# Kernel optimization log

Hardware: AMD Instinct MI355X
Metric: run time of the kernel (lower is better)

The kernel has to match this reference:

```python
import jax, jax.numpy as jnp
import numpy as np

N = 50000
E = 1600000
F_IN = 503
F_H = 128
NEG_SLOPE = 0.2


def setup_inputs() -> dict:
    key = jax.random.key(0)
    ks = jax.random.split(key, 24)
    s = 0.05
    inp = {
        "x": jax.random.normal(ks[0], (N, F_IN), jnp.float32),
        "edge_index": jax.random.randint(ks[1], (2, E), 0, N, jnp.int64),
        "edge_attr": jax.random.uniform(ks[2], (E, 1), jnp.float32),
        "input_mask": jax.random.uniform(ks[3], (N, 1), jnp.float32),
        # GATConv layer 1 (in=503, out=128, heads=1, edge_dim=1)
        "W1": jax.random.normal(ks[4], (F_IN, F_H), jnp.float32) * s,
        "b1": jnp.zeros((F_H,), jnp.float32),
        "as1": jax.random.normal(ks[5], (F_H,), jnp.float32) * s,
        "ad1": jax.random.normal(ks[6], (F_H,), jnp.float32) * s,
        "We1": jax.random.normal(ks[7], (1, F_H), jnp.float32) * s,
        "ae1": jax.random.normal(ks[8], (F_H,), jnp.float32) * s,
        # GATConv layer 2 (in=128, out=128)
        "W2": jax.random.normal(ks[9], (F_H, F_H), jnp.float32) * s,
        "b2": jnp.zeros((F_H,), jnp.float32),
        "as2": jax.random.normal(ks[10], (F_H,), jnp.float32) * s,
        "ad2": jax.random.normal(ks[11], (F_H,), jnp.float32) * s,
        "We2": jax.random.normal(ks[12], (1, F_H), jnp.float32) * s,
        "ae2": jax.random.normal(ks[13], (F_H,), jnp.float32) * s,
        # edge/node heads
        "Wb": jax.random.normal(ks[14], (F_H, 1), jnp.float32) * s,
        "bb": jnp.zeros((1,), jnp.float32),
        "Ww": jax.random.normal(ks[15], (F_H, 1), jnp.float32) * s,
        "bw": jnp.zeros((1,), jnp.float32),
    }
    return inp


def _gat_conv(x, src, dst, ea, W, b, a_src_vec, a_dst_vec, We, a_edge_vec):
    """PyG GATConv, heads=1, add_self_loops=True, fill_value='mean'."""
    n = x.shape[0]
    loop = jnp.arange(n)
    # self-loop edge attrs = mean of incoming edge attrs (0 if none)
    deg = jax.ops.segment_sum(jnp.ones(dst.shape, ea.dtype), dst, num_segments=n)
    ea_loop = jax.ops.segment_sum(ea, dst, num_segments=n) / jnp.maximum(deg, 1.0)[:, None]
    s = jnp.concatenate([src, loop])
    d = jnp.concatenate([dst, loop])
    ea2 = jnp.concatenate([ea, ea_loop], axis=0)  # [E+N, 1]

    h = x @ W                              # [N, F_H]
    a_s = h @ a_src_vec                    # [N]
    a_d = h @ a_dst_vec                    # [N]
    a_e = (ea2 @ We) @ a_edge_vec          # [E+N]

    alpha = jax.nn.leaky_relu(a_s[s] + a_d[d] + a_e, NEG_SLOPE)
    # scatter-softmax over destination neighborhoods (every node has a self loop)
    m = jax.lax.stop_gradient(jax.ops.segment_max(alpha, d, num_segments=n))
    ex = jnp.exp(alpha - m[d])
    den = jax.ops.segment_sum(ex, d, num_segments=n)
    coef = ex / den[d]                     # [E+N]

    out = jax.ops.segment_sum(coef[:, None] * h[s], d, num_segments=n)
    return out + b


def reference(x, edge_index, edge_attr, input_mask,
              W1, b1, as1, ad1, We1, ae1,
              W2, b2, as2, ad2, We2, ae2,
              Wb, bb, Ww, bw):
    src, dst = edge_index[0], edge_index[1]
    h = jax.nn.relu(_gat_conv(x, src, dst, edge_attr, W1, b1, as1, ad1, We1, ae1))
    h = jax.nn.relu(_gat_conv(h, src, dst, edge_attr, W2, b2, as2, ad2, We2, ae2))
    b_out = (h @ Wb + bb) * input_mask          # [N, 1]
    # directed graph: is_directed() is True, so use all edges
    w = ((h[src] + h[dst]) * 0.5) @ Ww + bw     # [E, 1]
    return (w, b_out)
```

## Files before the change

### kernel.cpp

```cpp
#include <hip/hip_runtime.h>
#include <hip/hip_fp16.h>

#define FH 128
#define NEG_SLOPE 0.2f
#define GBM 64
#define GBK 64
#define HT 1024
#define TB 8
#define NWMAX 12512
#define XLS 515


typedef _Float16 f16x8 __attribute__((ext_vector_type(8)));
typedef float f32x4 __attribute__((ext_vector_type(4)));

__global__ __launch_bounds__(HT) void hist_kernel(const int* __restrict__ ei,
                                                  unsigned short* __restrict__ hist,
                                                  int E, int N) {
  __shared__ unsigned int lh[NWMAX];
  const int b = blockIdx.x, tid = threadIdx.x;
  const int nw = (N + 3) >> 2;
  for (int j = tid; j < nw; j += HT) lh[j] = 0u;
  __syncthreads();
  const int i0 = b * (HT * TB) + tid * TB;
  if (i0 + TB <= E) {
    int4 da = *(const int4*)&ei[E + i0];
    int4 db = *(const int4*)&ei[E + i0 + 4];
    int dv[8] = {da.x, da.y, da.z, da.w, db.x, db.y, db.z, db.w};
    #pragma unroll
    for (int k = 0; k < 8; k++)
      atomicAdd(&lh[dv[k] >> 2], 1u << ((dv[k] & 3) * 8));
  } else {
    for (int i = i0; i < E; i++) {
      int d = ei[E + i];
      atomicAdd(&lh[d >> 2], 1u << ((d & 3) * 8));
    }
  }
  __syncthreads();
  unsigned short* hb = hist + (size_t)b * N;
  for (int j = tid; j < nw; j += HT) {
    unsigned v = lh[j];
    int bin = j * 4;
    if (bin + 3 < N) {
      ushort4 o;
      o.x = v & 255u; o.y = (v >> 8) & 255u; o.z = (v >> 16) & 255u; o.w = v >> 24;
      *(ushort4*)&hb[bin] = o;
    } else {
      for (int k = 0; k < 4 && bin + k < N; k++) hb[bin + k] = (v >> (k * 8)) & 255u;
    }
  }
}

__global__ void colscan_kernel(unsigned short* __restrict__ hist,
                               int* __restrict__ cnt, int N, int NBr) {
  int bin = blockIdx.x * 256 + threadIdx.x;
  if (bin >= N) return;
  int s = 0, b = 0;
  for (; b + 8 <= NBr; b += 8) {
    int t[8];
    #pragma unroll
    for (int k = 0; k < 8; k++) t[k] = hist[(size_t)(b + k) * N + bin];
    #pragma unroll
    for (int k = 0; k < 8; k++) {
      hist[(size_t)(b + k) * N + bin] = (unsigned short)s;
      s += t[k];
    }
  }
  for (; b < NBr; b++) {
    int t = hist[(size_t)b * N + bin];
    hist[(size_t)b * N + bin] = (unsigned short)s;
    s += t;
  }
  cnt[bin] = s;
}

__global__ void scan_blocksum(const int* __restrict__ deg, int* __restrict__ bsum, int n) {
  __shared__ int sm[256];
  int i = blockIdx.x * 256 + threadIdx.x;
  sm[threadIdx.x] = (i < n) ? deg[i] : 0;
  __syncthreads();
  for (int off = 128; off > 0; off >>= 1) {
    if (threadIdx.x < off) sm[threadIdx.x] += sm[threadIdx.x + off];
    __syncthreads();
  }
  if (threadIdx.x == 0) bsum[blockIdx.x] = sm[0];
}

__global__ void scan_bsum(int* __restrict__ bsum, int nb, int* __restrict__ rowptr, int N) {
  __shared__ int sm[1024];
  int t = threadIdx.x;
  int v = (t < nb) ? bsum[t] : 0;
  sm[t] = v;
  __syncthreads();
  for (int off = 1; off < 1024; off <<= 1) {
    int u = (t >= off) ? sm[t - off] : 0;
    __syncthreads();
    sm[t] += u;
    __syncthreads();
  }
  if (t < nb) bsum[t] = sm[t] - v;
  if (t == 1023) rowptr[N] = sm[1023];
}

__global__ void scan_final(const int* __restrict__ deg, const int* __restrict__ bsum,
                           int* __restrict__ rowptr, int n) {
  __shared__ int sm[256];
  int i = blockIdx.x * 256 + threadIdx.x;
  int v = (i < n) ? deg[i] : 0;
  sm[threadIdx.x] = v;
  __syncthreads();
  for (int off = 1; off < 256; off <<= 1) {
    int u = (threadIdx.x >= off) ? sm[threadIdx.x - off] : 0;
    __syncthreads();
    sm[threadIdx.x] += u;
    __syncthreads();
  }
  if (i < n) rowptr[i] = bsum[blockIdx.x] + sm[threadIdx.x] - v;
}

__global__ __launch_bounds__(HT) void place_kernel(const int* __restrict__ ei,
                                                   const float* __restrict__ ea,
                                                   const int* __restrict__ rowptr,
                                                   const unsigned short* __restrict__ off,
                                                   unsigned int* __restrict__ pack,
                                                   int E, int N) {
  __shared__ unsigned int lc[NWMAX];
  const int b = blockIdx.x, tid = threadIdx.x;
  const int nw = (N + 3) >> 2;
  for (int j = tid; j < nw; j += HT) lc[j] = 0u;
  __syncthreads();
  const unsigned short* __restrict__ ob = off + (size_t)b * N;
  const int i0 = b * (HT * TB) + tid * TB;
  if (i0 + TB <= E) {
    int4 sa = *(const int4*)&ei[i0];
    int4 sb = *(const int4*)&ei[i0 + 4];
    int4 da = *(const int4*)&ei[E + i0];
    int4 db = *(const int4*)&ei[E + i0 + 4];
    float4 aa = *(const float4*)&ea[i0];
    float4 ab = *(const float4*)&ea[i0 + 4];
    int sv[8] = {sa.x, sa.y, sa.z, sa.w, sb.x, sb.y, sb.z, sb.w};
    int dv[8] = {da.x, da.y, da.z, da.w, db.x, db.y, db.z, db.w};
    float av[8] = {aa.x, aa.y, aa.z, aa.w, ab.x, ab.y, ab.z, ab.w};
    unsigned rr[8];
    #pragma unroll
    for (int k = 0; k < 8; k++)
      rr[k] = atomicAdd(&lc[dv[k] >> 2], 1u << ((dv[k] & 3) * 8));
    int pos[8];
    #pragma unroll
    for (int k = 0; k < 8; k++)
      pos[k] = rowptr[dv[k]] + (int)ob[dv[k]] + (int)((rr[k] >> ((dv[k] & 3) * 8)) & 255u);
    #pragma unroll
    for (int k = 0; k < 8; k++)
      pack[pos[k]] = ((unsigned)sv[k] << 16) | __half_as_ushort(__float2half(av[k]));
  } else {
    for (int i = i0; i < E; i++) {
      int d = ei[E + i];
      unsigned r = atomicAdd(&lc[d >> 2], 1u << ((d & 3) * 8));
      int local = (r >> ((d & 3) * 8)) & 255;
      int pos = rowptr[d] + (int)ob[d] + local;
      pack[pos] = ((unsigned)ei[i] << 16) | __half_as_ushort(__float2half(ea[i]));
    }
  }
}

__global__ void cvec_kernel(const float* __restrict__ We1, const float* __restrict__ ae1,
                            const float* __restrict__ We2, const float* __restrict__ ae2,
                            float* __restrict__ cv) {
  int l = threadIdx.x;
  float s1 = We1[l] * ae1[l] + We1[l + 64] * ae1[l + 64];
  float s2 = We2[l] * ae2[l] + We2[l + 64] * ae2[l + 64];
  for (int off = 32; off; off >>= 1) { s1 += __shfl_down(s1, off); s2 += __shfl_down(s2, off); }
  if (l == 0) { cv[0] = s1; cv[1] = s2; }
}

__global__ void wcvt_kernel(const float* __restrict__ W, __half* __restrict__ Wt,
                            int K, int Kpad, int perm) {
  int idx = blockIdx.x * 256 + threadIdx.x;
  if (idx >= 128 * Kpad) return;
  int n = idx / Kpad, p = idx - n * Kpad;
  int k = perm ? ((p & 7) * 16 + (p >> 3)) : p;
  Wt[idx] = (k < K) ? __float2half(W[(size_t)k * 128 + n]) : __float2half(0.f);
}

__global__ __launch_bounds__(256) void xpack_kernel(const float* __restrict__ X,
                                                    __half* __restrict__ A16,
                                                    int K, int Kpad) {
  __shared__ float Ls[16 * XLS];
  const int mg = blockIdx.x, tid = threadIdx.x;
  const int nq = Kpad >> 3;
  const int total = 16 * K;
  const float* __restrict__ Xb = X + (size_t)mg * total;
  for (int i = tid; i < total; i += 256) {
    int row = i / K;
    Ls[row * XLS + (i - row * K)] = Xb[i];
  }
  {
    int npad = 16 * (Kpad - K);
    for (int i = tid; i < npad; i += 256) {
      int row = i / (Kpad - K);
      Ls[row * XLS + K + (i - row * (Kpad - K))] = 0.f;
    }
  }
  __syncthreads();
  _Float16* dst = (_Float16*)A16 + (size_t)mg * nq * 128;
  const int nfr = nq * 16;
  for (int c = tid; c < nfr; c += 256) {
    int q = c >> 4, r = c & 15;
    const float* src = &Ls[r * XLS + q * 8];
    f16x8 v;
    #pragma unroll
    for (int j = 0; j < 8; j++) v[j] = (_Float16)src[j];
    *(f16x8*)&dst[(size_t)c * 8] = v;
  }
}

__global__ __launch_bounds__(256, 4) void mfma_gemm_kernel(
    const __half* __restrict__ A16_, const __half* __restrict__ Wt_,
    const float* __restrict__ avs, const float* __restrict__ avd,
    __half* __restrict__ H16, float* __restrict__ a_s, float* __restrict__ a_d,
    int M, int Kpad) {
  __shared__ _Float16 Bl[2 * 8 * 64 * 8];
  const _Float16* __restrict__ A16 = (const _Float16*)A16_;
  const _Float16* __restrict__ Wt  = (const _Float16*)Wt_;
  const int tid  = threadIdx.x;
  const int lane = tid & 63;
  const int w    = tid >> 6;
  const int m0   = blockIdx.x * GBM;
  const int nq   = Kpad >> 3;

  f32x4 acc[8];
  #pragma unroll
  for (int i = 0; i < 8; i++) acc[i] = (f32x4){0.f, 0.f, 0.f, 0.f};

  const int mgc = min(m0 / 16 + w, M / 16 - 1);
  const _Float16* __restrict__ Abase =
      A16 + (size_t)mgc * nq * 128 + (lane >> 4) * 128 + (lane & 15) * 8;

  const int sg = tid & 7, snb = tid >> 3;

  for (int k0 = 0; k0 < Kpad; k0 += GBK) {
    #pragma unroll
    for (int i = 0; i < 4; i++) {
      int n = snb + 32 * i;
      f16x8 v = *(const f16x8*)(Wt + (size_t)n * Kpad + k0 + sg * 8);
      int kt = sg >> 2, nt = n >> 4;
      int fl = (n & 15) + (sg & 3) * 16;
      *(f16x8*)&Bl[((kt * 8 + nt) * 64 + fl) * 8] = v;
    }
    __syncthreads();
    #pragma unroll
    for (int kt = 0; kt < 2; kt++) {
      f16x8 af = *(const f16x8*)(Abase + (size_t)k0 * 16 + kt * 512);
      #pragma unroll
      for (int nt = 0; nt < 8; nt++) {
        f16x8 bf = *(const f16x8*)&Bl[((kt * 8 + nt) * 64 + lane) * 8];
        acc[nt] = __builtin_amdgcn_mfma_f32_16x16x32_f16(af, bf, acc[nt], 0, 0, 0);
      }
    }
    __syncthreads();
  }

  const int rbase = m0 + w * 16 + (lane >> 4) * 4;
  const int col   = lane & 15;
  float as_v[8], ad_v[8];
  #pragma unroll
  for (int nt = 0; nt < 8; nt++) {
    as_v[nt] = avs[nt * 16 + col];
    ad_v[nt] = avd[nt * 16 + col];
  }
  #pragma unroll
  for (int r = 0; r < 4; r++) {
    int gm = rbase + r;
    float ps = 0.f, pd = 0.f;
    #pragma unroll
    for (int nt = 0; nt < 8; nt++) {
      ps += acc[nt][r] * as_v[nt];
      pd += acc[nt][r] * ad_v[nt];
    }
    #pragma unroll
    for (int msk = 1; msk < 16; msk <<= 1) {
      ps += __shfl_xor(ps, msk);
      pd += __shfl_xor(pd, msk);
    }
    if (gm < M) {
      __half2 h0 = __floats2half2_rn(acc[0][r], acc[1][r]);
      __half2 h1 = __floats2half2_rn(acc[2][r], acc[3][r]);
      __half2 h2 = __floats2half2_rn(acc[4][r], acc[5][r]);
      __half2 h3 = __floats2half2_rn(acc[6][r], acc[7][r]);
      uint4 u;
      u.x = *(unsigned*)&h0; u.y = *(unsigned*)&h1;
      u.z = *(unsigned*)&h2; u.w = *(unsigned*)&h3;
      *(uint4*)&H16[(size_t)gm * FH + col * 8] = u;
      if (col == 0) { a_s[gm] = ps; a_d[gm] = pd; }
    }
  }
}

template<int OUTP>
__global__ __launch_bounds__(256) void agg_kernel(
    const __half* __restrict__ H16, const int* __restrict__ rowptr,
    const unsigned int* __restrict__ pack,
    const float* __restrict__ a_s, const float* __restrict__ a_d,
    const float* __restrict__ cv, int cidx,
    const float* __restrict__ bias,
    __half* __restrict__ HoutP,
    const float* __restrict__ Wb, const float* __restrict__ bb,
    const float* __restrict__ Ww, const float* __restrict__ mask,
    float* __restrict__ bout, float* __restrict__ pbuf, int N) {
  const int node = (blockIdx.x * 256 + threadIdx.x) >> 6;
  const int lane = threadIdx.x & 63;
  const int slot = lane >> 4, sl = lane & 15;
  if (node >= N) return;
  const _Float16* __restrict__ Hh = (const _Float16*)H16;
  const float c   = cv[cidx];
  const float adn = a_d[node];
  const int beg = rowptr[node], end = rowptr[node + 1];

  float acc[8] = {0.f, 0.f, 0.f, 0.f, 0.f, 0.f, 0.f, 0.f};
  float accB[8] = {0.f, 0.f, 0.f, 0.f, 0.f, 0.f, 0.f, 0.f};
  float den = 0.f, ea_tot = 0.f, denB = 0.f, eaB = 0.f;

  int p = beg + slot;
  for (; p + 4 < end; p += 8) {
    unsigned w0 = pack[p], w1 = pack[p + 4];
    int s0 = w0 >> 16, s1 = w1 >> 16;
    float e0 = __half2float(__ushort_as_half((unsigned short)(w0 & 0xffff)));
    float e1 = __half2float(__ushort_as_half((unsigned short)(w1 & 0xffff)));
    float as0 = a_s[s0], as1 = a_s[s1];
    f16x8 h0 = *(const f16x8*)(Hh + (size_t)s0 * FH + sl * 8);
    f16x8 h1 = *(const f16x8*)(Hh + (size_t)s1 * FH + sl * 8);
    float al0 = as0 + adn + c * e0;
    float al1 = as1 + adn + c * e1;
    al0 = fmaxf(al0, NEG_SLOPE * al0);
    al1 = fmaxf(al1, NEG_SLOPE * al1);
    float ex0 = __expf(al0), ex1 = __expf(al1);
    ea_tot += e0; eaB += e1;
    den += ex0; denB += ex1;
    #pragma unroll
    for (int j = 0; j < 8; j++) {
      acc[j]  += ex0 * (float)h0[j];
      accB[j] += ex1 * (float)h1[j];
    }
  }
  for (; p < end; p += 4) {
    unsigned w0 = pack[p];
    int s0 = w0 >> 16;
    float e0 = __half2float(__ushort_as_half((unsigned short)(w0 & 0xffff)));
    float al = a_s[s0] + adn + c * e0;
    al = fmaxf(al, NEG_SLOPE * al);
    float ex = __expf(al);
    f16x8 h = *(const f16x8*)(Hh + (size_t)s0 * FH + sl * 8);
    ea_tot += e0;
    den += ex;
    #pragma unroll
    for (int j = 0; j < 8; j++) acc[j] += ex * (float)h[j];
  }
  den += denB; ea_tot += eaB;
  #pragma unroll
  for (int j = 0; j < 8; j++) acc[j] += accB[j];
  ea_tot += __shfl_xor(ea_tot, 16); ea_tot += __shfl_xor(ea_tot, 32);
  den    += __shfl_xor(den,    16); den    += __shfl_xor(den,    32);
  #pragma unroll
  for (int j = 0; j < 8; j++) {
    acc[j] += __shfl_xor(acc[j], 16);
    acc[j] += __shfl_xor(acc[j], 32);
  }
  {
    int dg = end - beg;
    float eal = ea_tot / fmaxf((float)dg, 1.f);
    float al = a_s[node] + adn + c * eal;
    al = fmaxf(al, NEG_SLOPE * al);
    float ex = __expf(al);
    f16x8 h = *(const f16x8*)(Hh + (size_t)node * FH + sl * 8);
    den += ex;
    #pragma unroll
    for (int j = 0; j < 8; j++) acc[j] += ex * (float)h[j];
  }
  if (slot == 0) {
    float inv = 1.f / den;
    float v[8];
    #pragma unroll
    for (int j = 0; j < 8; j++)
      v[j] = fmaxf(acc[j] * inv + bias[j * 16 + sl], 0.f);
    if (OUTP) {
      f16x8 o;
      #pragma unroll
      for (int j = 0; j < 8; j++) o[j] = (_Float16)v[j];
      int mg = node >> 4, r = node & 15;
      *(f16x8*)((_Float16*)HoutP + (((size_t)mg * 16 + sl) * 16 + r) * 8) = o;
    } else {
      float sb = 0.f, sw = 0.f;
      #pragma unroll
      for (int j = 0; j < 8; j++) {
        int f = j * 16 + sl;
        sb += v[j] * Wb[f];
        sw += v[j] * Ww[f];
      }
      #pragma unroll
      for (int m = 1; m < 16; m <<= 1) {
        sb += __shfl_xor(sb, m);
        sw += __shfl_xor(sw, m);
      }
      if (sl == 0) {
        bout[node] = (sb + bb[0]) * mask[node];
        pbuf[node] = sw;
      }
    }
  }
}

__global__ void edge_head_kernel(const int* __restrict__ ei, const float* __restrict__ p,
                                 const float* __restrict__ bw, float* __restrict__ w, int E) {
  int base = (blockIdx.x * 256 + threadIdx.x) * 4;
  if (base >= E) return;
  float b = bw[0];
  if (base + 4 <= E) {
    int4 s = *(const int4*)&ei[base];
    int4 d = *(const int4*)&ei[E + base];
    float4 o;
    o.x = 0.5f * (p[s.x] + p[d.x]) + b;
    o.y = 0.5f * (p[s.y] + p[d.y]) + b;
    o.z = 0.5f * (p[s.z] + p[d.z]) + b;
    o.w = 0.5f * (p[s.w] + p[d.w]) + b;
    *(float4*)&w[base] = o;
  } else {
    for (int e = base; e < E; e++)
      w[e] = 0.5f * (p[ei[e]] + p[ei[E + e]]) + b;
  }
}

extern "C" void kernel_launch(void* const* d_in, const int* in_sizes, int n_in,
                              void* d_out, int out_size, void* d_ws, size_t ws_size,
                              hipStream_t stream) {
  (void)n_in; (void)out_size; (void)ws_size;
  const float* x    = (const float*)d_in[0];
  const int*   ei   = (const int*)  d_in[1];
  const float* ea   = (const float*)d_in[2];
  const float* mask = (const float*)d_in[3];
  const float* W1   = (const float*)d_in[4];
  const float* b1   = (const float*)d_in[5];
  const float* as1  = (const float*)d_in[6];
  const float* ad1  = (const float*)d_in[7];
  const float* We1  = (const float*)d_in[8];
  const float* ae1  = (const float*)d_in[9];
  const float* W2   = (const float*)d_in[10];
  const float* b2   = (const float*)d_in[11];
  const float* as2  = (const float*)d_in[12];
  const float* ad2  = (const float*)d_in[13];
  const float* We2  = (const float*)d_in[14];
  const float* ae2  = (const float*)d_in[15];
  const float* Wb   = (const float*)d_in[16];
  const float* bb   = (const float*)d_in[17];
  const float* Ww   = (const float*)d_in[18];
  const float* bw   = (const float*)d_in[19];

  const int N  = in_sizes[3];
  const int E  = in_sizes[1] / 2;
  const int K1 = in_sizes[0] / N;
  const int K1p = (K1 + GBK - 1) & ~(GBK - 1);
  const int NBr = (E + HT * TB - 1) / (HT * TB);
  const int NT  = N / 16;

  char* ws = (char*)d_ws;
  size_t off0 = 0;
  auto alloc = [&](size_t bytes) -> char* {
    char* q = ws + off0;
    off0 = (off0 + bytes + 255) & ~(size_t)255;
    return q;
  };
  int*   cnt    = (int*)  alloc((size_t)N * 4);
  int*   rowptr = (int*)  alloc((size_t)(N + 1) * 4);
  int*   bsum   = (int*)  alloc(1024 * 4);
  size_t uszA = (size_t)NBr * N * 2;
  size_t uszB = (size_t)NT * (K1p / 8) * 256;
  char*  uni  = alloc(uszA > uszB ? uszA : uszB);
  unsigned short* hist = (unsigned short*)uni;
  __half* XA16 = (__half*)uni;
  __half* HB16 = (__half*)uni;
  unsigned int* pack = (unsigned int*)alloc((size_t)E * 4);
  float* a_s    = (float*)alloc((size_t)N * 4);
  float* a_d    = (float*)alloc((size_t)N * 4);
  __half* H16   = (__half*)alloc((size_t)N * FH * 2);
  float* pbuf   = (float*)alloc((size_t)N * 4);
  float* cv     = (float*)alloc(8);
  __half* W1t   = (__half*)alloc((size_t)FH * K1p * 2);
  __half* W2t   = (__half*)alloc((size_t)FH * FH * 2);

  float* w_out = (float*)d_out;
  float* b_out = (float*)d_out + E;

  const int nb  = (N + 255) / 256;
  const int gb  = (N + GBM - 1) / GBM;
  const int ab  = (N + 3) / 4;
  const int eb4 = (E + 1023) / 1024;

  hist_kernel   <<<NBr, HT, 0, stream>>>(ei, hist, E, N);
  colscan_kernel<<<nb, 256, 0, stream>>>(hist, cnt, N, NBr);
  scan_blocksum <<<nb, 256, 0, stream>>>(cnt, bsum, N);
  scan_bsum     <<<1, 1024, 0, stream>>>(bsum, nb, rowptr, N);
  scan_final    <<<nb, 256, 0, stream>>>(cnt, bsum, rowptr, N);
  place_kernel  <<<NBr, HT, 0, stream>>>(ei, ea, rowptr, hist, pack, E, N);
  cvec_kernel   <<<1, 64, 0, stream>>>(We1, ae1, We2, ae2, cv);
  wcvt_kernel   <<<(128 * K1p + 255) / 256, 256, 0, stream>>>(W1, W1t, K1, K1p, 0);
  wcvt_kernel   <<<(128 * FH + 255) / 256, 256, 0, stream>>>(W2, W2t, FH, FH, 1);
  xpack_kernel  <<<NT, 256, 0, stream>>>(x, XA16, K1, K1p);

  mfma_gemm_kernel<<<gb, 256, 0, stream>>>(XA16, W1t, as1, ad1, H16, a_s, a_d, N, K1p);
  agg_kernel<1><<<ab, 256, 0, stream>>>(H16, rowptr, pack, a_s, a_d, cv, 0, b1,
                                        HB16, nullptr, nullptr, nullptr, nullptr,
                                        nullptr, nullptr, N);
  mfma_gemm_kernel<<<gb, 256, 0, stream>>>(HB16, W2t, as2, ad2, H16, a_s, a_d, N, FH);
  agg_kernel<0><<<ab, 256, 0, stream>>>(H16, rowptr, pack, a_s, a_d, cv, 1, b2,
                                        nullptr, Wb, bb, Ww, mask, b_out, pbuf, N);
  edge_head_kernel<<<eb4, 256, 0, stream>>>(ei, pbuf, bw, w_out, E);
}
```

Measured before the change: 269.3 us.

## Unroll aggregation gather loop 4x, merge weight conversions, use nontemporal pack stores

```diff
diff --git a/kernel.cpp b/kernel.cpp
--- a/kernel.cpp
+++ b/kernel.cpp
@@ -151,14 +151,16 @@
       pos[k] = rowptr[dv[k]] + (int)ob[dv[k]] + (int)((rr[k] >> ((dv[k] & 3) * 8)) & 255u);
     #pragma unroll
     for (int k = 0; k < 8; k++)
-      pack[pos[k]] = ((unsigned)sv[k] << 16) | __half_as_ushort(__float2half(av[k]));
+      __builtin_nontemporal_store(
+        ((unsigned)sv[k] << 16) | __half_as_ushort(__float2half(av[k])), &pack[pos[k]]);
   } else {
     for (int i = i0; i < E; i++) {
       int d = ei[E + i];
       unsigned r = atomicAdd(&lc[d >> 2], 1u << ((d & 3) * 8));
       int local = (r >> ((d & 3) * 8)) & 255;
       int pos = rowptr[d] + (int)ob[d] + local;
-      pack[pos] = ((unsigned)ei[i] << 16) | __half_as_ushort(__float2half(ea[i]));
+      __builtin_nontemporal_store(
+        ((unsigned)ei[i] << 16) | __half_as_ushort(__float2half(ea[i])), &pack[pos]);
     }
   }
 }
@@ -173,13 +175,22 @@
   if (l == 0) { cv[0] = s1; cv[1] = s2; }
 }
 
-__global__ void wcvt_kernel(const float* __restrict__ W, __half* __restrict__ Wt,
-                            int K, int Kpad, int perm) {
+__global__ void wcvt_kernel(const float* __restrict__ W1, __half* __restrict__ W1t,
+                            int K1, int K1p,
+                            const float* __restrict__ W2, __half* __restrict__ W2t) {
   int idx = blockIdx.x * 256 + threadIdx.x;
-  if (idx >= 128 * Kpad) return;
-  int n = idx / Kpad, p = idx - n * Kpad;
-  int k = perm ? ((p & 7) * 16 + (p >> 3)) : p;
-  Wt[idx] = (k < K) ? __float2half(W[(size_t)k * 128 + n]) : __float2half(0.f);
+  int n1 = 128 * K1p;
+  if (idx < n1) {
+    int n = idx / K1p, k = idx - n * K1p;
+    W1t[idx] = (k < K1) ? __float2half(W1[(size_t)k * 128 + n]) : __float2half(0.f);
+  } else {
+    int j = idx - n1;
+    if (j < 128 * 128) {
+      int n = j >> 7, p = j & 127;
+      int k = (p & 7) * 16 + (p >> 3);
+      W2t[j] = __float2half(W2[(size_t)k * 128 + n]);
+    }
+  }
 }
 
 __global__ __launch_bounds__(256) void xpack_kernel(const float* __restrict__ X,
@@ -321,25 +332,35 @@
   float den = 0.f, ea_tot = 0.f, denB = 0.f, eaB = 0.f;
 
   int p = beg + slot;
-  for (; p + 4 < end; p += 8) {
-    unsigned w0 = pack[p], w1 = pack[p + 4];
-    int s0 = w0 >> 16, s1 = w1 >> 16;
+  for (; p + 12 < end; p += 16) {
+    unsigned w0 = pack[p],     w1 = pack[p + 4];
+    unsigned w2 = pack[p + 8], w3 = pack[p + 12];
+    int s0 = w0 >> 16, s1 = w1 >> 16, s2 = w2 >> 16, s3 = w3 >> 16;
     float e0 = __half2float(__ushort_as_half((unsigned short)(w0 & 0xffff)));
     float e1 = __half2float(__ushort_as_half((unsigned short)(w1 & 0xffff)));
-    float as0 = a_s[s0], as1 = a_s[s1];
+    float e2 = __half2float(__ushort_as_half((unsigned short)(w2 & 0xffff)));
+    float e3 = __half2float(__ushort_as_half((unsigned short)(w3 & 0xffff)));
+    float as0 = a_s[s0], as1 = a_s[s1], as2 = a_s[s2], as3 = a_s[s3];
     f16x8 h0 = *(const f16x8*)(Hh + (size_t)s0 * FH + sl * 8);
     f16x8 h1 = *(const f16x8*)(Hh + (size_t)s1 * FH + sl * 8);
+    f16x8 h2 = *(const f16x8*)(Hh + (size_t)s2 * FH + sl * 8);
+    f16x8 h3 = *(const f16x8*)(Hh + (size_t)s3 * FH + sl * 8);
     float al0 = as0 + adn + c * e0;
     float al1 = as1 + adn + c * e1;
+    float al2 = as2 + adn + c * e2;
+    float al3 = as3 + adn + c * e3;
     al0 = fmaxf(al0, NEG_SLOPE * al0);
     al1 = fmaxf(al1, NEG_SLOPE * al1);
+    al2 = fmaxf(al2, NEG_SLOPE * al2);
+    al3 = fmaxf(al3, NEG_SLOPE * al3);
     float ex0 = __expf(al0), ex1 = __expf(al1);
-    ea_tot += e0; eaB += e1;
-    den += ex0; denB += ex1;
+    float ex2 = __expf(al2), ex3 = __expf(al3);
+    ea_tot += e0 + e2; eaB += e1 + e3;
+    den += ex0 + ex2; denB += ex1 + ex3;
     #pragma unroll
     for (int j = 0; j < 8; j++) {
-      acc[j]  += ex0 * (float)h0[j];
-      accB[j] += ex1 * (float)h1[j];
+      acc[j]  += ex0 * (float)h0[j] + ex2 * (float)h2[j];
+      accB[j] += ex1 * (float)h1[j] + ex3 * (float)h3[j];
     }
   }
   for (; p < end; p += 4) {
@@ -493,6 +514,7 @@
   const int gb  = (N + GBM - 1) / GBM;
   const int ab  = (N + 3) / 4;
   const int eb4 = (E + 1023) / 1024;
+  const int wcb = (128 * K1p + 128 * 128 + 255) / 256;
 
   hist_kernel   <<<NBr, HT, 0, stream>>>(ei, hist, E, N);
   colscan_kernel<<<nb, 256, 0, stream>>>(hist, cnt, N, NBr);
@@ -501,8 +523,7 @@
   scan_final    <<<nb, 256, 0, stream>>>(cnt, bsum, rowptr, N);
   place_kernel  <<<NBr, HT, 0, stream>>>(ei, ea, rowptr, hist, pack, E, N);
   cvec_kernel   <<<1, 64, 0, stream>>>(We1, ae1, We2, ae2, cv);
-  wcvt_kernel   <<<(128 * K1p + 255) / 256, 256, 0, stream>>>(W1, W1t, K1, K1p, 0);
-  wcvt_kernel   <<<(128 * FH + 255) / 256, 256, 0, stream>>>(W2, W2t, FH, FH, 1);
+  wcvt_kernel   <<<wcb, 256, 0, stream>>>(W1, W1t, K1, K1p, W2, W2t);
   xpack_kernel  <<<NT, 256, 0, stream>>>(x, XA16, K1, K1p);
 
   mfma_gemm_kernel<<<gb, 256, 0, stream>>>(XA16, W1t, as1, ad1, H16, a_s, a_d, N, K1p);
```

New measurement: 294.5 us. +9.3%, slower.
